# Optimization experiments

Measured on AMD Instinct MI355X. Metric: run time of the kernel, lower is better.

The kernel has to match this reference:

```python
import jax, jax.numpy as jnp
import numpy as np

CTX = 2048
D_IN = 1024
D_OUT = 1024
BATCH = 8


def setup_inputs() -> dict:
    key = jax.random.key(0)
    k1, k2, k3, k4 = jax.random.split(key, 4)
    x = jax.random.normal(k1, (BATCH, CTX, D_IN), dtype=jnp.float32)
    # nn.Linear weight is [out, in]; store pre-transposed as [in, out] for x @ W
    Wk = jax.random.normal(k2, (D_IN, D_OUT), dtype=jnp.float32) * (1.0 / np.sqrt(D_IN))
    Wq = jax.random.normal(k3, (D_IN, D_OUT), dtype=jnp.float32) * (1.0 / np.sqrt(D_IN))
    Wv = jax.random.normal(k4, (D_IN, D_OUT), dtype=jnp.float32) * (1.0 / np.sqrt(D_IN))
    return {"x": x, "Wq": Wq, "Wk": Wk, "Wv": Wv}


def reference(x, Wq, Wk, Wv):
    # projections: [b, s, d_out]
    q = jnp.einsum('bsi,io->bso', x, Wq)
    k = jnp.einsum('bsi,io->bso', x, Wk)
    v = jnp.einsum('bsi,io->bso', x, Wv)
    s = q.shape[1]
    scale = 1.0 / jnp.sqrt(jnp.asarray(q.shape[-1], q.dtype))
    att = jnp.einsum('bqd,bkd->bqk', q, k) * scale  # [b, s, s]
    # additive causal mask: 0 on/below diagonal, -inf above
    causal = jnp.tril(jnp.ones((s, s), dtype=bool))
    att = jnp.where(causal, att, -jnp.inf)
    att = jax.nn.softmax(att, axis=-1)
    return jnp.einsum('bqk,bkd->bqd', att, v)
```

## Files before the change

### kernel.cpp

```cpp
#include <hip/hip_runtime.h>
#include <stdint.h>

typedef unsigned short u16;
typedef short bf16x8 __attribute__((ext_vector_type(8)));
typedef float f32x4 __attribute__((ext_vector_type(4)));

#define CTX 2048
#define DIN 1024
#define DOUT 1024
#define NB 8

__device__ __forceinline__ u16 f2bf(float f) {
  uint32_t u = __builtin_bit_cast(uint32_t, f);
  u += 0x7FFFu + ((u >> 16) & 1u);
  return (u16)(u >> 16);
}

__device__ __forceinline__ void gld_lds16(const u16* g, const u16* lds) {
  __builtin_amdgcn_global_load_lds(
      (const __attribute__((address_space(1))) uint32_t*)(unsigned long long)(const void*)g,
      (__attribute__((address_space(3))) uint32_t*)(uint32_t)(unsigned long long)(const void*)lds,
      16, 0, 0);
}

#define SBAR() asm volatile("s_barrier" ::: "memory")
#define VMCNT4() asm volatile("s_waitcnt vmcnt(4)" ::: "memory")
#define VMCNT0() asm volatile("s_waitcnt vmcnt(0)" ::: "memory")

template <typename EPI>
__device__ __forceinline__ void gemm256(const u16* __restrict__ A, int lda,
                                        const u16* __restrict__ Bt, int ldb,
                                        int m0, int n0, int K, EPI&& epi) {
  __shared__ __align__(16) u16 lds[65536];

  const int t = threadIdx.x;
  const int lane = t & 63;
  const int w = t >> 6;
  const int wm = w >> 2;
  const int wn = w & 3;
  const int l15 = lane & 15;
  const int l16 = lane >> 4;
  const int nkt = K >> 6;
  const int bf0 = (wn & 1) * 4;

  f32x4 acc[8][4];
#pragma unroll
  for (int i = 0; i < 8; ++i)
#pragma unroll
    for (int j = 0; j < 4; ++j) acc[i][j] = {0.f, 0.f, 0.f, 0.f};

  const u16* gA0 = A + (size_t)(m0 + w * 16 + l15) * lda + l16 * 8;
  const u16* gA1 = gA0 + (size_t)128 * lda;
  const u16* gB0 = Bt + (size_t)(n0 + w * 16 + l15) * ldb + l16 * 8;
  const u16* gB1 = gB0 + (size_t)128 * ldb;

  auto STAGEH = [&](int bb, int rr, const u16* g) {
    u16* d = lds + (((bb * 4 + rr) * 16) + w * 2) * 512;
    gld_lds16(g, d);
    gld_lds16(g + 32, d + 512);
  };

  STAGEH(0, 0, gA0);
  STAGEH(0, 1, gA1);
  STAGEH(0, 2, gB0);
  STAGEH(0, 3, gB1);
  if (nkt > 1) {
    STAGEH(1, 0, gA0 + 64);
    STAGEH(1, 1, gA1 + 64);
  }
  VMCNT4();
  SBAR();

  bf16x8 arLo[4][2], arHi[4][2], br[2][2];

  {
    if (1 < nkt) STAGEH(1, 2, gB0 + 64);
    const u16* bufA = lds + ((0 * 4 + wm) * 16) * 512 + lane * 8;
    const u16* bufB = lds + ((0 * 4 + 2 + (wn >> 1)) * 16) * 512 + lane * 8;
#pragma unroll
    for (int fr = 0; fr < 4; ++fr)
#pragma unroll
      for (int ks = 0; ks < 2; ++ks)
        arLo[fr][ks] = *reinterpret_cast<const bf16x8*>(bufA + (fr * 2 + ks) * 512);
#pragma unroll
    for (int nc = 0; nc < 2; ++nc)
#pragma unroll
      for (int ks = 0; ks < 2; ++ks)
        br[nc][ks] = *reinterpret_cast<const bf16x8*>(bufB + ((bf0 + nc) * 2 + ks) * 512);
    SBAR();
  }

  auto kbody = [&](int T, int b) {
    const u16* bufA = lds + ((b * 4 + wm) * 16) * 512 + lane * 8;
    const u16* bufB = lds + ((b * 4 + 2 + (wn >> 1)) * 16) * 512 + lane * 8;
    const u16* bufAn = lds + (((b ^ 1) * 4 + wm) * 16) * 512 + lane * 8;
    const u16* bufBn = lds + (((b ^ 1) * 4 + 2 + (wn >> 1)) * 16) * 512 + lane * 8;

    if (T + 1 < nkt) STAGEH(b ^ 1, 3, gB1 + (size_t)(T + 1) * 64);
    __builtin_amdgcn_s_setprio(1);
#pragma unroll
    for (int fr = 0; fr < 4; ++fr)
#pragma unroll
      for (int nc = 0; nc < 2; ++nc)
#pragma unroll
        for (int ks = 0; ks < 2; ++ks)
          acc[fr][nc] = __builtin_amdgcn_mfma_f32_16x16x32_bf16(arLo[fr][ks], br[nc][ks],
                                                                acc[fr][nc], 0, 0, 0);
    __builtin_amdgcn_s_setprio(0);
#pragma unroll
    for (int fr = 0; fr < 4; ++fr)
#pragma unroll
      for (int ks = 0; ks < 2; ++ks)
        arHi[fr][ks] = *reinterpret_cast<const bf16x8*>(bufA + ((fr + 4) * 2 + ks) * 512);
    SBAR();

    if (T + 2 < nkt) STAGEH(b, 0, gA0 + (size_t)(T + 2) * 64);
    __builtin_amdgcn_s_setprio(1);
#pragma unroll
    for (int fr = 0; fr < 4; ++fr)
#pragma unroll
      for (int nc = 0; nc < 2; ++nc)
#pragma unroll
        for (int ks = 0; ks < 2; ++ks)
          acc[4 + fr][nc] = __builtin_amdgcn_mfma_f32_16x16x32_bf16(arHi[fr][ks], br[nc][ks],
                                                                    acc[4 + fr][nc], 0, 0, 0);
    __builtin_amdgcn_s_setprio(0);
#pragma unroll
    for (int nc = 0; nc < 2; ++nc)
#pragma unroll
      for (int ks = 0; ks < 2; ++ks)
        br[nc][ks] = *reinterpret_cast<const bf16x8*>(bufB + ((bf0 + 2 + nc) * 2 + ks) * 512);
    SBAR();

    if (T + 2 < nkt) STAGEH(b, 1, gA1 + (size_t)(T + 2) * 64);
    __builtin_amdgcn_s_setprio(1);
#pragma unroll
    for (int fr = 0; fr < 4; ++fr)
#pragma unroll
      for (int nc = 0; nc < 2; ++nc)
#pragma unroll
        for (int ks = 0; ks < 2; ++ks)
          acc[4 + fr][2 + nc] = __builtin_amdgcn_mfma_f32_16x16x32_bf16(arHi[fr][ks], br[nc][ks],
                                                                        acc[4 + fr][2 + nc], 0, 0, 0);
    __builtin_amdgcn_s_setprio(0);
    if (T + 2 < nkt) {
      VMCNT4();
    } else {
      VMCNT0();
    }
    SBAR();

    if (T + 2 < nkt) STAGEH(b, 2, gB0 + (size_t)(T + 2) * 64);
    __builtin_amdgcn_s_setprio(1);
#pragma unroll
    for (int fr = 0; fr < 4; ++fr)
#pragma unroll
      for (int nc = 0; nc < 2; ++nc)
#pragma unroll
        for (int ks = 0; ks < 2; ++ks)
          acc[fr][2 + nc] = __builtin_amdgcn_mfma_f32_16x16x32_bf16(arLo[fr][ks], br[nc][ks],
                                                                    acc[fr][2 + nc], 0, 0, 0);
    __builtin_amdgcn_s_setprio(0);
    if (T + 1 < nkt) {
#pragma unroll
      for (int fr = 0; fr < 4; ++fr)
#pragma unroll
        for (int ks = 0; ks < 2; ++ks)
          arLo[fr][ks] = *reinterpret_cast<const bf16x8*>(bufAn + (fr * 2 + ks) * 512);
#pragma unroll
      for (int nc = 0; nc < 2; ++nc)
#pragma unroll
        for (int ks = 0; ks < 2; ++ks)
          br[nc][ks] = *reinterpret_cast<const bf16x8*>(bufBn + ((bf0 + nc) * 2 + ks) * 512);
    }
    SBAR();
  };

  for (int TT = 0; TT < nkt; TT += 2) {
    kbody(TT, 0);
    kbody(TT + 1, 1);
  }

  epi(acc, wm * 128 + l16 * 4, wn * 64 + l15);
}

__global__ __launch_bounds__(256) void k_cvt_x(const float* __restrict__ x,
                                               u16* __restrict__ xb) {
  const int idx = (blockIdx.x * 256 + threadIdx.x) * 4;
  const float4 v = *reinterpret_cast<const float4*>(x + idx);
  ushort4 o;
  o.x = f2bf(v.x); o.y = f2bf(v.y); o.z = f2bf(v.z); o.w = f2bf(v.w);
  *reinterpret_cast<ushort4*>(xb + idx) = o;
}

__global__ __launch_bounds__(256) void k_cvt_wt(const float* __restrict__ W,
                                                u16* __restrict__ Wt) {
  __shared__ u16 tile[64][65];
  const int bc = blockIdx.x;
  const int tr0 = (bc >> 4) * 64;
  const int tc0 = (bc & 15) * 64;
  const int t = threadIdx.x;
  const int col = t & 63, rr = t >> 6;
#pragma unroll
  for (int p = 0; p < 16; ++p) {
    const int row = rr * 16 + p;
    tile[row][col] = f2bf(W[(size_t)(tr0 + row) * DOUT + tc0 + col]);
  }
  __syncthreads();
#pragma unroll
  for (int p = 0; p < 16; ++p) {
    const int row = rr * 16 + p;
    Wt[(size_t)(tc0 + row) * DIN + tr0 + col] = tile[col][row];
  }
}

__global__ __launch_bounds__(512, 2) void k_proj(const u16* __restrict__ xb,
                                                 const u16* __restrict__ Wt,
                                                 u16* __restrict__ qkb,
                                                 u16* __restrict__ vT) {
  const int wg = (blockIdx.x & 7) * 96 + (blockIdx.x >> 3);
  const int m0 = (wg / 12) * 256, n0 = (wg % 12) * 256;
  gemm256(xb, DIN, Wt, DIN, m0, n0, DIN,
          [&](const f32x4(&acc)[8][4], int r0, int c0) {
            if (n0 < 2 * DOUT) {
#pragma unroll
              for (int fr = 0; fr < 8; ++fr)
#pragma unroll
                for (int nc = 0; nc < 4; ++nc) {
                  const int r = m0 + r0 + fr * 16;
                  const int c = n0 + c0 + nc * 16;
#pragma unroll
                  for (int i = 0; i < 4; ++i)
                    qkb[(size_t)(r + i) * 2048 + c] = f2bf(acc[fr][nc][i]);
                }
            } else {
              const int b = m0 >> 11;
              const int sl = (m0 & (CTX - 1)) + r0;
              u16* C = vT + (size_t)b * DOUT * CTX;
#pragma unroll
              for (int fr = 0; fr < 8; ++fr)
#pragma unroll
                for (int nc = 0; nc < 4; ++nc) {
                  const int d = n0 - 2 * DOUT + c0 + nc * 16;
                  const int s = sl + fr * 16;
                  ushort4 o;
                  o.x = f2bf(acc[fr][nc][0]);
                  o.y = f2bf(acc[fr][nc][1]);
                  o.z = f2bf(acc[fr][nc][2]);
                  o.w = f2bf(acc[fr][nc][3]);
                  *reinterpret_cast<ushort4*>(C + (size_t)d * CTX + s) = o;
                }
            }
          });
}

__global__ __launch_bounds__(512, 2) void k_score(const u16* __restrict__ qkb,
                                                  float* __restrict__ S) {
  const int u = (blockIdx.x & 7) * 36 + (blockIdx.x >> 3);
  const int b = u / 36, v = u % 36;
  int it = 0;
  while ((it + 1) * (it + 2) / 2 <= v) ++it;
  const int jt = v - it * (it + 1) / 2;
  const u16* Aq = qkb + (size_t)b * CTX * 2048;
  float* C = S + ((size_t)b << 22);
  const int m0 = it * 256, n0 = jt * 256;
  gemm256(Aq, 2048, Aq + 1024, 2048, m0, n0, DOUT,
          [&](const f32x4(&acc)[8][4], int r0, int c0) {
#pragma unroll
            for (int fr = 0; fr < 8; ++fr)
#pragma unroll
              for (int nc = 0; nc < 4; ++nc) {
                const int r = m0 + r0 + fr * 16;
                const int c = n0 + c0 + nc * 16;
#pragma unroll
                for (int i = 0; i < 4; ++i)
                  C[(size_t)(r + i) * CTX + c] = acc[fr][nc][i] * 0.03125f;
              }
          });
}

__global__ __launch_bounds__(256) void k_softmax(float* __restrict__ Sws) {
  const int row = blockIdx.x;
  const int b = row >> 11, i = row & (CTX - 1);
  const float* srow = Sws + ((size_t)b << 22) + ((size_t)i << 11);
  u16* prow = (u16*)(Sws + ((size_t)b << 22)) + ((size_t)i << 12);
  const int t = threadIdx.x;
  const int j0 = t * 8;
  float vv[8];
  if (j0 <= i) {
    const float4 v0 = *reinterpret_cast<const float4*>(srow + j0);
    const float4 v1 = *reinterpret_cast<const float4*>(srow + j0 + 4);
    vv[0] = v0.x; vv[1] = v0.y; vv[2] = v0.z; vv[3] = v0.w;
    vv[4] = v1.x; vv[5] = v1.y; vv[6] = v1.z; vv[7] = v1.w;
  } else {
#pragma unroll
    for (int p = 0; p < 8; ++p) vv[p] = -3.0e38f;
  }
  float mx = -3.0e38f;
#pragma unroll
  for (int p = 0; p < 8; ++p) {
    vv[p] = (j0 + p <= i) ? vv[p] : -3.0e38f;
    mx = fmaxf(mx, vv[p]);
  }
#pragma unroll
  for (int off = 32; off > 0; off >>= 1) mx = fmaxf(mx, __shfl_xor(mx, off));
  __shared__ float redm[4], reds[4];
  const int lane = t & 63, wid = t >> 6;
  if (lane == 0) redm[wid] = mx;
  __syncthreads();
  mx = fmaxf(fmaxf(redm[0], redm[1]), fmaxf(redm[2], redm[3]));
  float e[8], s = 0.f;
#pragma unroll
  for (int p = 0; p < 8; ++p) {
    e[p] = __expf(vv[p] - mx);
    s += e[p];
  }
#pragma unroll
  for (int off = 32; off > 0; off >>= 1) s += __shfl_xor(s, off);
  if (lane == 0) reds[wid] = s;
  __syncthreads();
  s = reds[0] + reds[1] + reds[2] + reds[3];
  const float inv = 1.0f / s;
  ushort4 o0, o1;
  o0.x = (j0 + 0 <= i) ? f2bf(e[0] * inv) : (u16)0;
  o0.y = (j0 + 1 <= i) ? f2bf(e[1] * inv) : (u16)0;
  o0.z = (j0 + 2 <= i) ? f2bf(e[2] * inv) : (u16)0;
  o0.w = (j0 + 3 <= i) ? f2bf(e[3] * inv) : (u16)0;
  o1.x = (j0 + 4 <= i) ? f2bf(e[4] * inv) : (u16)0;
  o1.y = (j0 + 5 <= i) ? f2bf(e[5] * inv) : (u16)0;
  o1.z = (j0 + 6 <= i) ? f2bf(e[6] * inv) : (u16)0;
  o1.w = (j0 + 7 <= i) ? f2bf(e[7] * inv) : (u16)0;
  *reinterpret_cast<ushort4*>(prow + j0) = o0;
  *reinterpret_cast<ushort4*>(prow + j0 + 4) = o1;
}

__global__ __launch_bounds__(512, 2) void k_out(const float* __restrict__ Sws,
                                                const u16* __restrict__ vT,
                                                float* __restrict__ out) {
  const int idx = blockIdx.x;
  const int it = 7 - (idx >> 5);
  const int b = (idx >> 2) & 7;
  const int nt = idx & 3;
  const u16* P = (const u16*)(Sws + ((size_t)b << 22));
  const u16* Bt = vT + (size_t)b * DOUT * CTX;
  float* C = out + (size_t)b * CTX * DOUT;
  const int m0 = it * 256, n0 = nt * 256;
  gemm256(P, 2 * CTX, Bt, CTX, m0, n0, (it + 1) * 256,
          [&](const f32x4(&acc)[8][4], int r0, int c0) {
#pragma unroll
            for (int fr = 0; fr < 8; ++fr)
#pragma unroll
              for (int nc = 0; nc < 4; ++nc) {
                const int r = m0 + r0 + fr * 16;
                const int c = n0 + c0 + nc * 16;
#pragma unroll
                for (int i = 0; i < 4; ++i)
                  C[(size_t)(r + i) * DOUT + c] = acc[fr][nc][i];
              }
          });
}

extern "C" void kernel_launch(void* const* d_in, const int* in_sizes, int n_in,
                              void* d_out, int out_size, void* d_ws, size_t ws_size,
                              hipStream_t stream) {
  (void)in_sizes; (void)n_in; (void)out_size; (void)ws_size;
  const float* x = (const float*)d_in[0];
  const float* Wq = (const float*)d_in[1];
  const float* Wk = (const float*)d_in[2];
  const float* Wv = (const float*)d_in[3];
  float* out = (float*)d_out;
  uint8_t* ws = (uint8_t*)d_ws;

  float* S = (float*)ws;
  u16* xb = (u16*)ws;
  u16* Wt_all = (u16*)(ws + 33554432ull);
  u16* qkb = (u16*)(ws + 134217728ull);
  u16* vT = (u16*)(ws + 201326592ull);

  k_cvt_x<<<16384, 256, 0, stream>>>(x, xb);
  k_cvt_wt<<<256, 256, 0, stream>>>(Wq, Wt_all);
  k_cvt_wt<<<256, 256, 0, stream>>>(Wk, Wt_all + 1024ull * 1024);
  k_cvt_wt<<<256, 256, 0, stream>>>(Wv, Wt_all + 2048ull * 1024);
  k_proj<<<768, 512, 0, stream>>>(xb, Wt_all, qkb, vT);
  k_score<<<288, 512, 0, stream>>>(qkb, S);
  k_softmax<<<NB * CTX, 256, 0, stream>>>(S);
  k_out<<<256, 512, 0, stream>>>(S, vT, out);
}
```

Measured before the change: 311.8 us.

## Restructure GEMM k-loop into 4-phase schedule with explicit LDS waits and sched barriers

Reorganizes the 256x256 GEMM main loop so each k-tile starts by loading its own A-low/B fragments from LDS instead of prefetching the next tile's at the end of the previous iteration. Each of the four MFMA phases is now bracketed by barriers, an lgkmcnt(0) wait and a sched_barrier, and the global->LDS staging of B halves and A halves is reshuffled across phases. The aim is a cleaner, compiler-proof ordering of LDS reads, async copies and MFMAs. In exchange it adds more barriers and removes the cross-iteration register prefetch, which may expose LDS latency.

```diff
diff --git a/kernel.cpp b/kernel.cpp
--- a/kernel.cpp
+++ b/kernel.cpp
@@ -26,6 +26,8 @@
 #define SBAR() asm volatile("s_barrier" ::: "memory")
 #define VMCNT4() asm volatile("s_waitcnt vmcnt(4)" ::: "memory")
 #define VMCNT0() asm volatile("s_waitcnt vmcnt(0)" ::: "memory")
+#define LGKM0() asm volatile("s_waitcnt lgkmcnt(0)" ::: "memory")
+#define SCHED0() __builtin_amdgcn_sched_barrier(0)
 
 template <typename EPI>
 __device__ __forceinline__ void gemm256(const u16* __restrict__ A, int lda,
@@ -73,30 +75,24 @@
 
   bf16x8 arLo[4][2], arHi[4][2], br[2][2];
 
-  {
-    if (1 < nkt) STAGEH(1, 2, gB0 + 64);
-    const u16* bufA = lds + ((0 * 4 + wm) * 16) * 512 + lane * 8;
-    const u16* bufB = lds + ((0 * 4 + 2 + (wn >> 1)) * 16) * 512 + lane * 8;
-#pragma unroll
-    for (int fr = 0; fr < 4; ++fr)
-#pragma unroll
-      for (int ks = 0; ks < 2; ++ks)
-        arLo[fr][ks] = *reinterpret_cast<const bf16x8*>(bufA + (fr * 2 + ks) * 512);
-#pragma unroll
-    for (int nc = 0; nc < 2; ++nc)
-#pragma unroll
-      for (int ks = 0; ks < 2; ++ks)
-        br[nc][ks] = *reinterpret_cast<const bf16x8*>(bufB + ((bf0 + nc) * 2 + ks) * 512);
-    SBAR();
-  }
-
   auto kbody = [&](int T, int b) {
     const u16* bufA = lds + ((b * 4 + wm) * 16) * 512 + lane * 8;
     const u16* bufB = lds + ((b * 4 + 2 + (wn >> 1)) * 16) * 512 + lane * 8;
-    const u16* bufAn = lds + (((b ^ 1) * 4 + wm) * 16) * 512 + lane * 8;
-    const u16* bufBn = lds + (((b ^ 1) * 4 + 2 + (wn >> 1)) * 16) * 512 + lane * 8;
-
-    if (T + 1 < nkt) STAGEH(b ^ 1, 3, gB1 + (size_t)(T + 1) * 64);
+
+#pragma unroll
+    for (int fr = 0; fr < 4; ++fr)
+#pragma unroll
+      for (int ks = 0; ks < 2; ++ks)
+        arLo[fr][ks] = *reinterpret_cast<const bf16x8*>(bufA + (fr * 2 + ks) * 512);
+#pragma unroll
+    for (int nc = 0; nc < 2; ++nc)
+#pragma unroll
+      for (int ks = 0; ks < 2; ++ks)
+        br[nc][ks] = *reinterpret_cast<const bf16x8*>(bufB + ((bf0 + nc) * 2 + ks) * 512);
+    if (T + 1 < nkt) STAGEH(b ^ 1, 2, gB0 + (size_t)(T + 1) * 64);
+    SBAR();
+    LGKM0();
+    SCHED0();
     __builtin_amdgcn_s_setprio(1);
 #pragma unroll
     for (int fr = 0; fr < 4; ++fr)
@@ -107,14 +103,17 @@
           acc[fr][nc] = __builtin_amdgcn_mfma_f32_16x16x32_bf16(arLo[fr][ks], br[nc][ks],
                                                                 acc[fr][nc], 0, 0, 0);
     __builtin_amdgcn_s_setprio(0);
+    SBAR();
+
 #pragma unroll
     for (int fr = 0; fr < 4; ++fr)
 #pragma unroll
       for (int ks = 0; ks < 2; ++ks)
         arHi[fr][ks] = *reinterpret_cast<const bf16x8*>(bufA + ((fr + 4) * 2 + ks) * 512);
-    SBAR();
-
-    if (T + 2 < nkt) STAGEH(b, 0, gA0 + (size_t)(T + 2) * 64);
+    if (T + 1 < nkt) STAGEH(b ^ 1, 3, gB1 + (size_t)(T + 1) * 64);
+    SBAR();
+    LGKM0();
+    SCHED0();
     __builtin_amdgcn_s_setprio(1);
 #pragma unroll
     for (int fr = 0; fr < 4; ++fr)
@@ -125,14 +124,17 @@
           acc[4 + fr][nc] = __builtin_amdgcn_mfma_f32_16x16x32_bf16(arHi[fr][ks], br[nc][ks],
                                                                     acc[4 + fr][nc], 0, 0, 0);
     __builtin_amdgcn_s_setprio(0);
+    SBAR();
+
 #pragma unroll
     for (int nc = 0; nc < 2; ++nc)
 #pragma unroll
       for (int ks = 0; ks < 2; ++ks)
         br[nc][ks] = *reinterpret_cast<const bf16x8*>(bufB + ((bf0 + 2 + nc) * 2 + ks) * 512);
-    SBAR();
-
-    if (T + 2 < nkt) STAGEH(b, 1, gA1 + (size_t)(T + 2) * 64);
+    if (T + 2 < nkt) STAGEH(b, 0, gA0 + (size_t)(T + 2) * 64);
+    SBAR();
+    LGKM0();
+    SCHED0();
     __builtin_amdgcn_s_setprio(1);
 #pragma unroll
     for (int fr = 0; fr < 4; ++fr)
@@ -142,36 +144,25 @@
         for (int ks = 0; ks < 2; ++ks)
           acc[4 + fr][2 + nc] = __builtin_amdgcn_mfma_f32_16x16x32_bf16(arHi[fr][ks], br[nc][ks],
                                                                         acc[4 + fr][2 + nc], 0, 0, 0);
+    __builtin_amdgcn_s_setprio(0);
+    SBAR();
+
+    if (T + 2 < nkt) STAGEH(b, 1, gA1 + (size_t)(T + 2) * 64);
+    SBAR();
+    __builtin_amdgcn_s_setprio(1);
+#pragma unroll
+    for (int fr = 0; fr < 4; ++fr)
+#pragma unroll
+      for (int nc = 0; nc < 2; ++nc)
+#pragma unroll
+        for (int ks = 0; ks < 2; ++ks)
+          acc[fr][2 + nc] = __builtin_amdgcn_mfma_f32_16x16x32_bf16(arLo[fr][ks], br[nc][ks],
+                                                                    acc[fr][2 + nc], 0, 0, 0);
     __builtin_amdgcn_s_setprio(0);
     if (T + 2 < nkt) {
       VMCNT4();
     } else {
       VMCNT0();
-    }
-    SBAR();
-
-    if (T + 2 < nkt) STAGEH(b, 2, gB0 + (size_t)(T + 2) * 64);
-    __builtin_amdgcn_s_setprio(1);
-#pragma unroll
-    for (int fr = 0; fr < 4; ++fr)
-#pragma unroll
-      for (int nc = 0; nc < 2; ++nc)
-#pragma unroll
-        for (int ks = 0; ks < 2; ++ks)
-          acc[fr][2 + nc] = __builtin_amdgcn_mfma_f32_16x16x32_bf16(arLo[fr][ks], br[nc][ks],
-                                                                    acc[fr][2 + nc], 0, 0, 0);
-    __builtin_amdgcn_s_setprio(0);
-    if (T + 1 < nkt) {
-#pragma unroll
-      for (int fr = 0; fr < 4; ++fr)
-#pragma unroll
-        for (int ks = 0; ks < 2; ++ks)
-          arLo[fr][ks] = *reinterpret_cast<const bf16x8*>(bufAn + (fr * 2 + ks) * 512);
-#pragma unroll
-      for (int nc = 0; nc < 2; ++nc)
-#pragma unroll
-        for (int ks = 0; ks < 2; ++ks)
-          br[nc][ks] = *reinterpret_cast<const bf16x8*>(bufBn + ((bf0 + nc) * 2 + ks) * 512);
     }
     SBAR();
   };
```

Result: no change. 313.0 us (+0.4%).

## Use 128x256 tiles with paired causal rows in PV GEMM, merge weight conversions

Applied to the files above, without the earlier changes.

The output (P·V) GEMM moves from 256x256 tiles to a new 128x256 GEMM with a triple-buffered 32-wide K pipeline. Each block handles two row tiles paired as (15-p, p) so the causal work per block is balanced. Occupancy rises to 4 blocks per CU through a smaller LDS footprint. The three weight-conversion launches are also merged into one kernel. The risk is lower arithmetic intensity per tile and more barrier overhead from the shorter K step.

```diff
diff --git a/kernel.cpp b/kernel.cpp
--- a/kernel.cpp
+++ b/kernel.cpp
@@ -25,6 +25,7 @@
 
 #define SBAR() asm volatile("s_barrier" ::: "memory")
 #define VMCNT4() asm volatile("s_waitcnt vmcnt(4)" ::: "memory")
+#define VMCNT3() asm volatile("s_waitcnt vmcnt(3)" ::: "memory")
 #define VMCNT0() asm volatile("s_waitcnt vmcnt(0)" ::: "memory")
 
 template <typename EPI>
@@ -184,6 +185,81 @@
   epi(acc, wm * 128 + l16 * 4, wn * 64 + l15);
 }
 
+template <typename EPI>
+__device__ __forceinline__ void gemm128x256(const u16* __restrict__ A, int lda,
+                                            const u16* __restrict__ Bt, int ldb,
+                                            int m0, int n0, int K, EPI&& epi) {
+  __shared__ __align__(16) u16 lds[36864];
+
+  const int t = threadIdx.x;
+  const int lane = t & 63;
+  const int w = t >> 6;
+  const int wm = w >> 2;
+  const int wn = w & 3;
+  const int l15 = lane & 15;
+  const int l16 = lane >> 4;
+  const int nkt = K >> 5;
+
+  f32x4 acc[4][4];
+#pragma unroll
+  for (int i = 0; i < 4; ++i)
+#pragma unroll
+    for (int j = 0; j < 4; ++j) acc[i][j] = {0.f, 0.f, 0.f, 0.f};
+
+  const u16* gA = A + (size_t)(m0 + w * 16 + l15) * lda + l16 * 8;
+  const u16* gB = Bt + (size_t)(n0 + w * 16 + l15) * ldb + l16 * 8;
+  const size_t ldJB = (size_t)128 * ldb;
+
+  auto STAGE = [&](int kbuf, int T) {
+    const size_t koff = (size_t)T * 32;
+    u16* base = lds + kbuf * 12288;
+    gld_lds16(gA + koff, base + w * 512);
+    gld_lds16(gB + koff, base + 4096 + w * 512);
+    gld_lds16(gB + koff + ldJB, base + 8192 + w * 512);
+  };
+
+  STAGE(0, 0);
+  STAGE(1, 1);
+  VMCNT3();
+  SBAR();
+
+  int cb = 0;
+  int sb = 2;
+  for (int T = 0; T < nkt; ++T) {
+    if (T + 2 < nkt) STAGE(sb, T + 2);
+
+    const u16* bufA = lds + cb * 12288 + (wm * 4) * 512 + lane * 8;
+    const u16* bufB = lds + cb * 12288 + 4096 + (wn * 4) * 512 + lane * 8;
+    bf16x8 ar[4], br[4];
+#pragma unroll
+    for (int fr = 0; fr < 4; ++fr)
+      ar[fr] = *reinterpret_cast<const bf16x8*>(bufA + fr * 512);
+#pragma unroll
+    for (int nc = 0; nc < 4; ++nc)
+      br[nc] = *reinterpret_cast<const bf16x8*>(bufB + nc * 512);
+
+    __builtin_amdgcn_s_setprio(1);
+#pragma unroll
+    for (int fr = 0; fr < 4; ++fr)
+#pragma unroll
+      for (int nc = 0; nc < 4; ++nc)
+        acc[fr][nc] = __builtin_amdgcn_mfma_f32_16x16x32_bf16(ar[fr], br[nc],
+                                                              acc[fr][nc], 0, 0, 0);
+    __builtin_amdgcn_s_setprio(0);
+    __builtin_amdgcn_sched_barrier(0);
+    if (T + 2 < nkt) {
+      VMCNT3();
+    } else {
+      VMCNT0();
+    }
+    SBAR();
+    cb = (cb == 2) ? 0 : cb + 1;
+    sb = (sb == 2) ? 0 : sb + 1;
+  }
+
+  epi(acc, wm * 64 + l16 * 4, wn * 64 + l15);
+}
+
 __global__ __launch_bounds__(256) void k_cvt_x(const float* __restrict__ x,
                                                u16* __restrict__ xb) {
   const int idx = (blockIdx.x * 256 + threadIdx.x) * 4;
@@ -193,10 +269,15 @@
   *reinterpret_cast<ushort4*>(xb + idx) = o;
 }
 
-__global__ __launch_bounds__(256) void k_cvt_wt(const float* __restrict__ W,
-                                                u16* __restrict__ Wt) {
+__global__ __launch_bounds__(256) void k_cvt_wt3(const float* __restrict__ Wq,
+                                                 const float* __restrict__ Wk,
+                                                 const float* __restrict__ Wv,
+                                                 u16* __restrict__ Wt_all) {
   __shared__ u16 tile[64][65];
-  const int bc = blockIdx.x;
+  const int sel = blockIdx.x >> 8;
+  const int bc = blockIdx.x & 255;
+  const float* W = (sel == 0) ? Wq : ((sel == 1) ? Wk : Wv);
+  u16* Wt = Wt_all + ((size_t)sel << 20);
   const int tr0 = (bc >> 4) * 64;
   const int tc0 = (bc & 15) * 64;
   const int t = threadIdx.x;
@@ -334,30 +415,36 @@
   *reinterpret_cast<ushort4*>(prow + j0 + 4) = o1;
 }
 
-__global__ __launch_bounds__(512, 2) void k_out(const float* __restrict__ Sws,
+__global__ __launch_bounds__(512, 4) void k_out(const float* __restrict__ Sws,
                                                 const u16* __restrict__ vT,
                                                 float* __restrict__ out) {
   const int idx = blockIdx.x;
-  const int it = 7 - (idx >> 5);
+  const int pp = idx >> 5;
   const int b = (idx >> 2) & 7;
   const int nt = idx & 3;
   const u16* P = (const u16*)(Sws + ((size_t)b << 22));
   const u16* Bt = vT + (size_t)b * DOUT * CTX;
   float* C = out + (size_t)b * CTX * DOUT;
-  const int m0 = it * 256, n0 = nt * 256;
-  gemm256(P, 2 * CTX, Bt, CTX, m0, n0, (it + 1) * 256,
-          [&](const f32x4(&acc)[8][4], int r0, int c0) {
-#pragma unroll
-            for (int fr = 0; fr < 8; ++fr)
-#pragma unroll
-              for (int nc = 0; nc < 4; ++nc) {
-                const int r = m0 + r0 + fr * 16;
-                const int c = n0 + c0 + nc * 16;
-#pragma unroll
-                for (int i = 0; i < 4; ++i)
-                  C[(size_t)(r + i) * DOUT + c] = acc[fr][nc][i];
-              }
-          });
+#pragma unroll 1
+  for (int s = 0; s < 2; ++s) {
+    const int it = s ? pp : (15 - pp);
+    const int m0 = it * 128, n0 = nt * 256;
+    gemm128x256(P, 2 * CTX, Bt, CTX, m0, n0, (it + 1) * 128,
+                [&](const f32x4(&acc)[4][4], int r0, int c0) {
+#pragma unroll
+                  for (int fr = 0; fr < 4; ++fr)
+#pragma unroll
+                    for (int nc = 0; nc < 4; ++nc) {
+                      const int r = m0 + r0 + fr * 16;
+                      const int c = n0 + c0 + nc * 16;
+#pragma unroll
+                      for (int i = 0; i < 4; ++i)
+                        C[(size_t)(r + i) * DOUT + c] = acc[fr][nc][i];
+                    }
+                });
+    VMCNT0();
+    SBAR();
+  }
 }
 
 extern "C" void kernel_launch(void* const* d_in, const int* in_sizes, int n_in,
@@ -378,9 +465,7 @@
   u16* vT = (u16*)(ws + 201326592ull);
 
   k_cvt_x<<<16384, 256, 0, stream>>>(x, xb);
-  k_cvt_wt<<<256, 256, 0, stream>>>(Wq, Wt_all);
-  k_cvt_wt<<<256, 256, 0, stream>>>(Wk, Wt_all + 1024ull * 1024);
-  k_cvt_wt<<<256, 256, 0, stream>>>(Wv, Wt_all + 2048ull * 1024);
+  k_cvt_wt3<<<768, 256, 0, stream>>>(Wq, Wk, Wv, Wt_all);
   k_proj<<<768, 512, 0, stream>>>(xb, Wt_all, qkb, vT);
   k_score<<<288, 512, 0, stream>>>(qkb, S);
   k_softmax<<<NB * CTX, 256, 0, stream>>>(S);
```

Result: faster. 294.6 us (-5.5%).
